# Optimization experiments

Hardware: AMD Instinct MI355X
Metric: run time of the kernel (lower is better)

## Reference

```python
import jax, jax.numpy as jnp
import numpy as np

N = 1024          # n_nodes
E = 32768         # n_edges (includes N self-loops)
EMBED = 256       # embed_dim
NHEAD = 8
NHID = EMBED // NHEAD  # 32
SLOPE = 0.2       # leaky_relu negative slope
NEG = -1e30       # mask value (finite to keep grads clean)


def setup_inputs() -> dict:
    key = jax.random.key(0)
    k1, k2, k3, k4, k5 = jax.random.split(key, 5)
    h = jax.random.normal(k1, (N, EMBED), dtype=jnp.float32)
    # self-loops first so every destination row has >=1 unmasked edge
    loops = jnp.stack([jnp.arange(N, dtype=jnp.int32)] * 2, axis=1)
    rnd = jax.random.randint(k2, (E - N, 2), 0, N, dtype=jnp.int32)
    edge_index = jnp.concatenate([loops, rnd], axis=0)  # [E, 2] = (r, c)
    W_l = jax.random.normal(k3, (EMBED, NHEAD * NHID), jnp.float32) / np.sqrt(EMBED).astype(np.float32)
    W_r = jax.random.normal(k4, (EMBED, NHEAD * NHID), jnp.float32) / np.sqrt(EMBED).astype(np.float32)
    attn_w = jax.random.normal(k5, (NHID,), jnp.float32) / np.sqrt(NHID).astype(np.float32)
    return {"h": h, "edge_index": edge_index, "W_l": W_l, "W_r": W_r, "attn_w": attn_w}


def reference(h, edge_index, W_l, W_r, attn_w):
    n = h.shape[0]
    g_l = (h @ W_l).reshape(n, NHEAD, NHID)  # [N, H, D]
    g_r = (h @ W_r).reshape(n, NHEAD, NHID)  # [N, H, D]
    # dense all-pairs GATv2 score: g_sum[i, j] = g_l[j] + g_r[i]
    # (matches g_l.repeat(n,1,1) + g_r.repeat_interleave(n, dim=0))
    g_sum = g_l[None, :, :, :] + g_r[:, None, :, :]            # [N, N, H, D]
    e = jnp.einsum('ijhd,d->ijh', jax.nn.leaky_relu(g_sum, SLOPE), attn_w)  # [N, N, H]
    # edge mask: keep only (r, c) pairs present in edge_index
    adj = jnp.zeros((n, n), dtype=bool).at[edge_index[:, 0], edge_index[:, 1]].set(True)
    e = jnp.where(adj[:, :, None], e, NEG)
    a = jax.nn.softmax(e, axis=1)                               # softmax over source nodes j
    # attention-weighted aggregation of source features, concat heads
    out = jnp.einsum('ijh,jhd->ihd', a, g_l).reshape(n, NHEAD * NHID)  # [N, EMBED]
    return out
```

## Files before the change

### kernel.cpp

```cpp
#include <hip/hip_runtime.h>
#include <hip/hip_bf16.h>
#include <stdint.h>

#define NN 1024
#define EMBED 256
#define NHEAD 8
#define NHID 32
#define SLOPE 0.2f
#define DEGMAX 64

template <int CTRL>
__device__ __forceinline__ float dpp_mov(float x) {
    int r = __builtin_amdgcn_update_dpp(0, __float_as_int(x), CTRL, 0xF, 0xF, true);
    return __int_as_float(r);
}
__device__ __forceinline__ float group32_sum(float v) {
    v += dpp_mov<0xB1>(v);
    v += dpp_mov<0x4E>(v);
    v += dpp_mov<0x141>(v);
    v += dpp_mov<0x140>(v);
    v += __shfl_xor(v, 16);
    return v;
}

__global__ __launch_bounds__(256) void k_prep(const float* __restrict__ h,
                                              const float* __restrict__ Wl,
                                              const float* __restrict__ Wr,
                                              const int* __restrict__ ei, int E,
                                              float* __restrict__ gl,
                                              float* __restrict__ gr,
                                              int* __restrict__ nbrg,
                                              int* __restrict__ cntg) {
    const int blk = blockIdx.x;
    const int t = threadIdx.x;

    if (blk < 128) {
        const int z  = blk & 1;
        const int bn = ((blk >> 1) & 3) * 64;
        const int bm = (blk >> 3) * 64;
        const float* W = z ? Wr : Wl;
        float* outg = z ? gr : gl;
        const int tx = t & 15;
        const int ty = t >> 4;

        __shared__ float As[16][68];
        __shared__ float Bs[16][68];

        float acc[4][4];
#pragma unroll
        for (int i = 0; i < 4; ++i)
#pragma unroll
            for (int j = 0; j < 4; ++j) acc[i][j] = 0.f;

        const int ar = t >> 2, ac = (t & 3) << 2;
        const int br = t >> 4, bc = (t & 15) << 2;
        const float* Ap = &h[(bm + ar) * EMBED + ac];
        const float* Bp = &W[br * EMBED + bn + bc];

        float4 a_reg = *reinterpret_cast<const float4*>(Ap);
        float4 b_reg = *reinterpret_cast<const float4*>(Bp);

        for (int k0 = 0; k0 < EMBED; k0 += 16) {
            As[ac + 0][ar] = a_reg.x; As[ac + 1][ar] = a_reg.y;
            As[ac + 2][ar] = a_reg.z; As[ac + 3][ar] = a_reg.w;
            Bs[br][bc + 0] = b_reg.x; Bs[br][bc + 1] = b_reg.y;
            Bs[br][bc + 2] = b_reg.z; Bs[br][bc + 3] = b_reg.w;
            __syncthreads();
            if (k0 + 16 < EMBED) {
                a_reg = *reinterpret_cast<const float4*>(Ap + k0 + 16);
                b_reg = *reinterpret_cast<const float4*>(Bp + (size_t)(k0 + 16) * EMBED);
            }
#pragma unroll
            for (int kk = 0; kk < 16; ++kk) {
                float4 av = *reinterpret_cast<const float4*>(&As[kk][ty * 4]);
                float4 bv = *reinterpret_cast<const float4*>(&Bs[kk][tx * 4]);
                float a[4] = {av.x, av.y, av.z, av.w};
                float b[4] = {bv.x, bv.y, bv.z, bv.w};
#pragma unroll
                for (int i = 0; i < 4; ++i)
#pragma unroll
                    for (int j = 0; j < 4; ++j) acc[i][j] += a[i] * b[j];
            }
            __syncthreads();
        }
#pragma unroll
        for (int i = 0; i < 4; ++i) {
            float4 v = make_float4(acc[i][0], acc[i][1], acc[i][2], acc[i][3]);
            *reinterpret_cast<float4*>(&outg[(bm + ty * 4 + i) * EMBED + bn + tx * 4]) = v;
        }
    } else {
        const int lo = (blk - 128) * 32;
        __shared__ unsigned int lads[1024];
#pragma unroll
        for (int u = 0; u < 4; ++u) lads[t + u * 256] = 0u;
        __syncthreads();

        const int4* ei4 = reinterpret_cast<const int4*>(ei);
        const int nvec = E >> 1;
        int base = 0;
        for (; base + 2048 <= nvec; base += 2048) {
#pragma unroll 8
            for (int u = 0; u < 8; ++u) {
                int4 v = ei4[base + u * 256 + t];
                int r0 = v.x - lo;
                if ((unsigned)r0 < 32u)
                    atomicOr(&lads[r0 * 32 + ((unsigned)v.y >> 5)], 1u << (v.y & 31));
                int r1 = v.z - lo;
                if ((unsigned)r1 < 32u)
                    atomicOr(&lads[r1 * 32 + ((unsigned)v.w >> 5)], 1u << (v.w & 31));
            }
        }
        for (int idx = base + t; idx < nvec; idx += 256) {
            int4 v = ei4[idx];
            int r0 = v.x - lo;
            if ((unsigned)r0 < 32u)
                atomicOr(&lads[r0 * 32 + ((unsigned)v.y >> 5)], 1u << (v.y & 31));
            int r1 = v.z - lo;
            if ((unsigned)r1 < 32u)
                atomicOr(&lads[r1 * 32 + ((unsigned)v.w >> 5)], 1u << (v.w & 31));
        }
        __syncthreads();

        const int wv = t >> 6, ln = t & 63;
        for (int rl = wv * 8; rl < wv * 8 + 8; ++rl) {
            unsigned int w = (ln < 32) ? lads[rl * 32 + ln] : 0u;
            int c = __popc(w);
            int pre = c;
#pragma unroll
            for (int d = 1; d < 32; d <<= 1) {
                int v = __shfl_up(pre, d);
                if (ln >= d) pre += v;
            }
            int tot = __shfl(pre, 31);
            int off = pre - c;
            if (ln == 0) cntg[lo + rl] = tot;
            while (w) {
                int b = __builtin_ctz(w);
                w &= w - 1;
                if (off < DEGMAX) nbrg[(lo + rl) * DEGMAX + off] = ln * 32 + b;
                ++off;
            }
        }
    }
}

__global__ __launch_bounds__(256) void k_attn(const float* __restrict__ gl,
                                              const float* __restrict__ gr,
                                              const int* __restrict__ nbrg,
                                              const int* __restrict__ cntg,
                                              const float* __restrict__ attn_w,
                                              float* __restrict__ out) {
    const int i = blockIdx.x;
    const int t = threadIdx.x;

    __shared__ int nbr_s[DEGMAX];
    __shared__ int cnt_sh;

    if (t == 0) cnt_sh = cntg[i];
    if (t < DEGMAX) nbr_s[t] = nbrg[i * DEGMAX + t];
    __syncthreads();

    const int cnt = cnt_sh;
    const float grv = gr[i * EMBED + t];
    const float aw = attn_w[t & 31];

    float m = -3e38f, s = 0.f, acc = 0.f;

    float g[4];
#pragma unroll
    for (int u = 0; u < 4; ++u) {
        int e = (u < cnt) ? u : cnt - 1;
        g[u] = gl[nbr_s[e] * EMBED + t];
    }

    for (int e0 = 0; e0 < cnt; e0 += 4) {
        float cg[4];
#pragma unroll
        for (int u = 0; u < 4; ++u) cg[u] = g[u];
#pragma unroll
        for (int u = 0; u < 4; ++u) {
            int e = e0 + 4 + u;
            e = (e < cnt) ? e : cnt - 1;
            g[u] = gl[nbr_s[e] * EMBED + t];
        }
        float p[4];
#pragma unroll
        for (int u = 0; u < 4; ++u) {
            float x = cg[u] + grv;
            p[u] = group32_sum((x > 0.f ? x : SLOPE * x) * aw);
        }
        float pm = p[0];
#pragma unroll
        for (int u = 1; u < 4; ++u)
            if (e0 + u < cnt) pm = fmaxf(pm, p[u]);
        float mn = fmaxf(m, pm);
        float sc = __expf(m - mn);
        float ev[4];
#pragma unroll
        for (int u = 0; u < 4; ++u)
            ev[u] = (e0 + u < cnt) ? __expf(p[u] - mn) : 0.f;
        s = s * sc + ((ev[0] + ev[1]) + (ev[2] + ev[3]));
        acc = acc * sc + ((ev[0] * cg[0] + ev[1] * cg[1]) + (ev[2] * cg[2] + ev[3] * cg[3]));
        m = mn;
    }
    out[i * EMBED + t] = acc / s;
}

extern "C" void kernel_launch(void* const* d_in, const int* in_sizes, int n_in,
                              void* d_out, int out_size, void* d_ws, size_t ws_size,
                              hipStream_t stream) {
    const float* h  = (const float*)d_in[0];
    const int*   ei = (const int*)d_in[1];
    const float* Wl = (const float*)d_in[2];
    const float* Wr = (const float*)d_in[3];
    const float* aw = (const float*)d_in[4];
    float* out = (float*)d_out;
    const int E = in_sizes[1] / 2;

    int* nbrg = (int*)d_ws;
    int* cntg = (int*)((char*)d_ws + NN * DEGMAX * 4);
    float* gl = (float*)((char*)d_ws + NN * DEGMAX * 4 + 4096);
    float* gr = gl + NN * EMBED;

    k_prep<<<160, 256, 0, stream>>>(h, Wl, Wr, ei, E, gl, gr, nbrg, cntg);
    k_attn<<<NN, 256, 0, stream>>>(gl, gr, nbrg, cntg, aw, out);
}
```

Baseline: 36.93 us.

## Compute projection GEMM with split-bf16 MFMA instead of scalar FP32 FMAs

Replaces the scalar FP32 register-tiled GEMM in the prep kernel with MFMA 16x16x32 bf16 instructions. Each operand is split into high and low bf16 parts, and three MFMAs per tile approximate FP32 accuracy. Tiles are staged in LDS as bf16 hi/lo arrays, which raises LDS use and adds conversion ALU work. It aims to cut GEMM time in the prep kernel, but the loads are no longer prefetched across k-tiles and the output stores are scalar.

Measured after the change: 36.84 us. Within noise of the previous version (-0.2%).

```diff
diff --git a/kernel.cpp b/kernel.cpp
--- a/kernel.cpp
+++ b/kernel.cpp
@@ -8,6 +8,18 @@
 #define NHID 32
 #define SLOPE 0.2f
 #define DEGMAX 64
+
+typedef __attribute__((ext_vector_type(8))) short short8;
+typedef __attribute__((ext_vector_type(4))) float f32x4;
+
+__device__ __forceinline__ unsigned short f32_to_bf16(float f) {
+    unsigned int u = __float_as_uint(f);
+    unsigned int r = (u + 0x7FFFu + ((u >> 16) & 1u)) >> 16;
+    return (unsigned short)r;
+}
+__device__ __forceinline__ float bf16_to_f32(unsigned short h) {
+    return __uint_as_float(((unsigned int)h) << 16);
+}
 
 template <int CTRL>
 __device__ __forceinline__ float dpp_mov(float x) {
@@ -40,54 +52,117 @@
         const int bm = (blk >> 3) * 64;
         const float* W = z ? Wr : Wl;
         float* outg = z ? gr : gl;
-        const int tx = t & 15;
-        const int ty = t >> 4;
-
-        __shared__ float As[16][68];
-        __shared__ float Bs[16][68];
-
-        float acc[4][4];
-#pragma unroll
-        for (int i = 0; i < 4; ++i)
-#pragma unroll
-            for (int j = 0; j < 4; ++j) acc[i][j] = 0.f;
-
-        const int ar = t >> 2, ac = (t & 3) << 2;
-        const int br = t >> 4, bc = (t & 15) << 2;
-        const float* Ap = &h[(bm + ar) * EMBED + ac];
-        const float* Bp = &W[br * EMBED + bn + bc];
-
-        float4 a_reg = *reinterpret_cast<const float4*>(Ap);
-        float4 b_reg = *reinterpret_cast<const float4*>(Bp);
-
-        for (int k0 = 0; k0 < EMBED; k0 += 16) {
-            As[ac + 0][ar] = a_reg.x; As[ac + 1][ar] = a_reg.y;
-            As[ac + 2][ar] = a_reg.z; As[ac + 3][ar] = a_reg.w;
-            Bs[br][bc + 0] = b_reg.x; Bs[br][bc + 1] = b_reg.y;
-            Bs[br][bc + 2] = b_reg.z; Bs[br][bc + 3] = b_reg.w;
+
+        __shared__ unsigned short Ah[64 * 72];
+        __shared__ unsigned short Al[64 * 72];
+        __shared__ unsigned short Bh[64 * 72];
+        __shared__ unsigned short Bl[64 * 72];
+
+        const int m_ld = t >> 2;
+        const int kq   = (t & 3) << 4;
+        const float* Ap = &h[(bm + m_ld) * EMBED + kq];
+        const int kp = t >> 3;
+        const int n0 = (t & 7) << 3;
+        const float* Bp = &W[(2 * kp) * EMBED + bn + n0];
+
+        const int wid = t >> 6, lane = t & 63;
+        const int wr = wid >> 1, wc = wid & 1;
+        const int l16 = lane & 15, g = lane >> 4;
+
+        f32x4 acc[2][2];
+#pragma unroll
+        for (int mi = 0; mi < 2; ++mi)
+#pragma unroll
+            for (int ni = 0; ni < 2; ++ni) acc[mi][ni] = (f32x4)(0.f);
+
+        for (int kt = 0; kt < 4; ++kt) {
+            const int K0 = kt * 64;
+            float4 a0 = *(const float4*)(Ap + K0);
+            float4 a1 = *(const float4*)(Ap + K0 + 4);
+            float4 a2 = *(const float4*)(Ap + K0 + 8);
+            float4 a3 = *(const float4*)(Ap + K0 + 12);
+            float4 b0 = *(const float4*)(Bp + (size_t)K0 * EMBED);
+            float4 b1 = *(const float4*)(Bp + (size_t)K0 * EMBED + 4);
+            float4 b2 = *(const float4*)(Bp + (size_t)(K0 + 1) * EMBED);
+            float4 b3 = *(const float4*)(Bp + (size_t)(K0 + 1) * EMBED + 4);
+
             __syncthreads();
-            if (k0 + 16 < EMBED) {
-                a_reg = *reinterpret_cast<const float4*>(Ap + k0 + 16);
-                b_reg = *reinterpret_cast<const float4*>(Bp + (size_t)(k0 + 16) * EMBED);
-            }
-#pragma unroll
-            for (int kk = 0; kk < 16; ++kk) {
-                float4 av = *reinterpret_cast<const float4*>(&As[kk][ty * 4]);
-                float4 bv = *reinterpret_cast<const float4*>(&Bs[kk][tx * 4]);
-                float a[4] = {av.x, av.y, av.z, av.w};
-                float b[4] = {bv.x, bv.y, bv.z, bv.w};
-#pragma unroll
-                for (int i = 0; i < 4; ++i)
-#pragma unroll
-                    for (int j = 0; j < 4; ++j) acc[i][j] += a[i] * b[j];
+
+            {
+                float av[16] = {a0.x, a0.y, a0.z, a0.w, a1.x, a1.y, a1.z, a1.w,
+                                a2.x, a2.y, a2.z, a2.w, a3.x, a3.y, a3.z, a3.w};
+                unsigned short hi[16], lo[16];
+#pragma unroll
+                for (int j = 0; j < 16; ++j) {
+                    hi[j] = f32_to_bf16(av[j]);
+                    lo[j] = f32_to_bf16(av[j] - bf16_to_f32(hi[j]));
+                }
+                const int base = m_ld * 72 + kq;
+#pragma unroll
+                for (int q = 0; q < 4; ++q) {
+                    *(ushort4*)&Ah[base + q * 4] =
+                        make_ushort4(hi[q*4], hi[q*4+1], hi[q*4+2], hi[q*4+3]);
+                    *(ushort4*)&Al[base + q * 4] =
+                        make_ushort4(lo[q*4], lo[q*4+1], lo[q*4+2], lo[q*4+3]);
+                }
+            }
+            {
+                float r0[8] = {b0.x, b0.y, b0.z, b0.w, b1.x, b1.y, b1.z, b1.w};
+                float r1[8] = {b2.x, b2.y, b2.z, b2.w, b3.x, b3.y, b3.z, b3.w};
+#pragma unroll
+                for (int j = 0; j < 8; ++j) {
+                    unsigned short h0 = f32_to_bf16(r0[j]);
+                    unsigned short h1 = f32_to_bf16(r1[j]);
+                    unsigned short l0 = f32_to_bf16(r0[j] - bf16_to_f32(h0));
+                    unsigned short l1 = f32_to_bf16(r1[j] - bf16_to_f32(h1));
+                    const int base = (n0 + j) * 72 + 2 * kp;
+                    *(unsigned int*)&Bh[base] = (unsigned int)h0 | ((unsigned int)h1 << 16);
+                    *(unsigned int*)&Bl[base] = (unsigned int)l0 | ((unsigned int)l1 << 16);
+                }
             }
             __syncthreads();
-        }
-#pragma unroll
-        for (int i = 0; i < 4; ++i) {
-            float4 v = make_float4(acc[i][0], acc[i][1], acc[i][2], acc[i][3]);
-            *reinterpret_cast<float4*>(&outg[(bm + ty * 4 + i) * EMBED + bn + tx * 4]) = v;
-        }
+
+#pragma unroll
+            for (int ks = 0; ks < 2; ++ks) {
+                const int kk = ks * 32 + g * 8;
+                short8 ah[2], al[2], bh[2], bl[2];
+#pragma unroll
+                for (int mi = 0; mi < 2; ++mi) {
+                    const int r = (wr * 32 + mi * 16 + l16) * 72 + kk;
+                    ah[mi] = *(const short8*)&Ah[r];
+                    al[mi] = *(const short8*)&Al[r];
+                }
+#pragma unroll
+                for (int ni = 0; ni < 2; ++ni) {
+                    const int r = (wc * 32 + ni * 16 + l16) * 72 + kk;
+                    bh[ni] = *(const short8*)&Bh[r];
+                    bl[ni] = *(const short8*)&Bl[r];
+                }
+#pragma unroll
+                for (int mi = 0; mi < 2; ++mi)
+#pragma unroll
+                    for (int ni = 0; ni < 2; ++ni) {
+                        acc[mi][ni] = __builtin_amdgcn_mfma_f32_16x16x32_bf16(
+                            ah[mi], bh[ni], acc[mi][ni], 0, 0, 0);
+                        acc[mi][ni] = __builtin_amdgcn_mfma_f32_16x16x32_bf16(
+                            ah[mi], bl[ni], acc[mi][ni], 0, 0, 0);
+                        acc[mi][ni] = __builtin_amdgcn_mfma_f32_16x16x32_bf16(
+                            al[mi], bh[ni], acc[mi][ni], 0, 0, 0);
+                    }
+            }
+        }
+
+#pragma unroll
+        for (int mi = 0; mi < 2; ++mi)
+#pragma unroll
+            for (int ni = 0; ni < 2; ++ni) {
+                const int col = bn + wc * 32 + ni * 16 + l16;
+#pragma unroll
+                for (int p = 0; p < 4; ++p) {
+                    const int row = bm + wr * 32 + mi * 16 + g * 4 + p;
+                    outg[row * EMBED + col] = acc[mi][ni][p];
+                }
+            }
     } else {
         const int lo = (blk - 128) * 32;
         __shared__ unsigned int lads[1024];
```
